# Kernel optimization log

Measured on AMD Instinct MI355X. Metric: run time of the kernel, lower is better.

## Reference

```python
import jax, jax.numpy as jnp
import numpy as np

N_GRAMS = 3
N_KERNELS = 11

def _kernel_mus(K):
    l = [1.0]
    if K == 1:
        return l
    bs = 2.0 / (K - 1)
    l.append(1.0 - bs / 2.0)
    for i in range(1, K - 1):
        l.append(l[i] - bs)
    return l

def _kernel_sigmas(K):
    if K == 1:
        return [0.001]
    bs = 2.0 / (K - 1)
    return [0.001] + [0.5 * bs] * (K - 1)

MU = jnp.asarray(_kernel_mus(N_KERNELS), jnp.float32)       # (K,)
SIGMA = jnp.asarray(_kernel_sigmas(N_KERNELS), jnp.float32)  # (K,)

def _conv_relu(x, w, b):
    # x: (B,E,L), w: (O,E,h); right-pad h-1 so output length == L (as ConstantPad1d((0,h-1)))
    h = w.shape[-1]
    y = jax.lax.conv_general_dilated(x, w, (1,), [(0, h - 1)], dimension_numbers=('NCH', 'OIH', 'NCH'))
    return jax.nn.relu(y + b[None, :, None]).transpose(0, 2, 1)  # (B,L,O)

def _cosine(a, b):
    # CosineMatrixAttention: normalize rows then matmul
    an = a / (jnp.linalg.norm(a, axis=-1, keepdims=True) + 1e-13)
    bn = b / (jnp.linalg.norm(b, axis=-1, keepdims=True) + 1e-13)
    return jnp.einsum('bqe,bde->bqd', an, bn)

def setup_inputs() -> dict:
    key = jax.random.key(0)
    ks = jax.random.split(key, 12)
    B, Lq, Ld, V, E, O = 128, 64, 512, 30000, 300, 128
    inp = {}
    inp['tokens_q'] = jax.random.randint(ks[0], (B, Lq), 0, V)
    inp['tokens_d'] = jax.random.randint(ks[1], (B, Ld), 0, V)
    inp['emb'] = jax.random.normal(ks[2], (V, E), jnp.float32) * 0.1
    for i, h in enumerate((1, 2, 3)):
        inp['conv_w%d' % h] = jax.random.normal(ks[3 + i], (O, E, h), jnp.float32) * (1.0 / np.sqrt(E * h))
        inp['conv_b%d' % h] = jnp.zeros((O,), jnp.float32)
    inp['fc_w'] = jax.random.normal(ks[9], (1, N_KERNELS * N_GRAMS * N_GRAMS), jnp.float32) * 0.1
    inp['fc_b'] = jnp.zeros((1,), jnp.float32)
    return inp

def reference(tokens_q, tokens_d, emb, conv_w1, conv_b1, conv_w2, conv_b2, conv_w3, conv_b3, fc_w, fc_b):
    qmask = (tokens_q > 0).astype(jnp.float32)  # (B,Lq)
    dmask = (tokens_d > 0).astype(jnp.float32)  # (B,Ld)
    qe = emb[tokens_q].transpose(0, 2, 1)  # (B,E,Lq)
    de = emb[tokens_d].transpose(0, 2, 1)  # (B,E,Ld)
    cws = [(conv_w1, conv_b1), (conv_w2, conv_b2), (conv_w3, conv_b3)]
    hq = [_conv_relu(qe, w, b) for w, b in cws]  # each (B,Lq,O)
    hd = [_conv_relu(de, w, b) for w, b in cws]  # each (B,Ld,O)
    pair_mask = qmask[:, :, None] * dmask[:, None, :]  # (B,Lq,Ld)
    mu = MU[None, None, None, :]
    sig = SIGMA[None, None, None, :]
    feats = []
    for q in range(N_GRAMS):
        for d in range(N_GRAMS):
            m = _cosine(hq[q], hd[d]) * pair_mask  # (B,Lq,Ld)
            rbf = jnp.exp(-jnp.square(m[..., None] - mu) / (2.0 * jnp.square(sig))) * pair_mask[..., None]
            qk = rbf.sum(axis=2)  # (B,Lq,K)
            logk = jnp.log(jnp.maximum(qk, 1e-10)) * 0.01
            # NOTE: original has a typo (loq_ vs log_) so the query mask is NOT applied before summing
            feats.append(logk.sum(axis=1))  # (B,K)
    cross = jnp.concatenate(feats, axis=-1)  # (B, K*G*G)
    return cross @ fc_w.T + fc_b  # (B,1)
```

## Files before the change

### kernel.cpp

```cpp
#include <hip/hip_runtime.h>
#include <hip/hip_bf16.h>

typedef __attribute__((ext_vector_type(8))) short short8;
typedef __attribute__((ext_vector_type(4))) float f32x4;

#define E_DIM 300
#define NCH   128
#define NOUT  384
#define NCHUNK 30

#define APITCH 656
#define OPITCH 792

__device__ __forceinline__ unsigned short f2bf(float f) {
    unsigned int u = __float_as_uint(f);
    u += 0x7FFFu + ((u >> 16) & 1u);
    return (unsigned short)(u >> 16);
}

__global__ void pack_wb(const float* __restrict__ w1, const float* __restrict__ w2,
                        const float* __restrict__ w3, unsigned short* __restrict__ Wp) {
    int idx = blockIdx.x * 256 + threadIdx.x;
    if (idx >= NCHUNK * NOUT * 32) return;
    int ke = idx & 31;
    int n  = (idx >> 5) % NOUT;
    int c  = idx / (32 * NOUT);
    int s  = c / 10;
    int e  = (c % 10) * 32 + ke;
    int g  = n >> 7, o = n & 127, h = g + 1;
    float v = 0.0f;
    if (e < E_DIM && s < h) {
        const float* w = (g == 0) ? w1 : ((g == 1) ? w2 : w3);
        v = w[(o * E_DIM + e) * h + s];
    }
    Wp[idx] = f2bf(v);
}

__launch_bounds__(512, 4)
__global__ void conv_mfma(const int* __restrict__ tokens_q, const int* __restrict__ tokens_d,
                          const float* __restrict__ emb, const unsigned short* __restrict__ Wp,
                          const float* __restrict__ b1, const float* __restrict__ b2,
                          const float* __restrict__ b3,
                          unsigned short* __restrict__ hq, unsigned short* __restrict__ hd) {
    __shared__ __align__(16) char lds[64 * OPITCH];
    __shared__ float nrm[64 * 3];

    int bx   = blockIdx.x;
    int b    = bx / 9;
    int tile = bx % 9;
    int isq  = (tile == 0);
    int L    = isq ? 64 : 512;
    int t0   = isq ? 0 : (tile - 1) * 64;
    const int* toks = isq ? (tokens_q + b * 64) : (tokens_d + b * 512);
    int tid  = threadIdx.x;
    int lane = tid & 63;
    int wn   = tid >> 6;
    int lr   = lane & 15;
    int lg   = lane >> 4;

    if (tid < 192) nrm[tid] = 0.0f;

    const unsigned short* __restrict__ wpB = Wp + (size_t)(wn * 16 + lr) * 32 + lg * 8;
    short8 bb[2][3];
    #pragma unroll
    for (int g = 0; g < 3; ++g) {
        bb[0][g] = *(const short8*)(wpB + (size_t)(0 * NOUT + g * 128) * 32);
        bb[1][g] = *(const short8*)(wpB + (size_t)(1 * NOUT + g * 128) * 32);
    }

    for (int i = tid; i < 66 * 80; i += 512) {
        int r   = i / 80;
        int f4  = i - r * 80;
        ushort4 u = {0, 0, 0, 0};
        int pos = t0 + r;
        if (f4 < 75 && pos < L) {
            int tk = toks[pos];
            float4 v = *(const float4*)(emb + (size_t)tk * E_DIM + f4 * 4);
            u.x = f2bf(v.x); u.y = f2bf(v.y); u.z = f2bf(v.z); u.w = f2bf(v.w);
        }
        *(ushort4*)(lds + r * APITCH + f4 * 8) = u;
    }
    __syncthreads();

    f32x4 acc[4][3];
    #pragma unroll
    for (int i = 0; i < 4; ++i)
        #pragma unroll
        for (int g = 0; g < 3; ++g) acc[i][g] = (f32x4){0.f, 0.f, 0.f, 0.f};

    const char* abase = lds + lr * APITCH + lg * 16;

    #pragma unroll
    for (int c = 0; c < NCHUNK; ++c) {
        const int S  = (c >= 20) ? 2 : ((c >= 10) ? 1 : 0);
        const int ec = c - S * 10;
        short8 a[4];
        #pragma unroll
        for (int i = 0; i < 4; ++i)
            a[i] = *(const short8*)(abase + (i * 16 + S) * APITCH + ec * 64);
        #pragma unroll
        for (int i = 0; i < 4; ++i)
            #pragma unroll
            for (int g = S; g < 3; ++g)
                acc[i][g] = __builtin_amdgcn_mfma_f32_16x16x32_bf16(a[i], bb[c & 1][g], acc[i][g], 0, 0, 0);
        if (c < NCHUNK - 2) {
            const int S2 = ((c + 2) >= 20) ? 2 : (((c + 2) >= 10) ? 1 : 0);
            #pragma unroll
            for (int g = S2; g < 3; ++g)
                bb[c & 1][g] = *(const short8*)(wpB + (size_t)((c + 2) * NOUT + g * 128) * 32);
        }
    }

    #pragma unroll
    for (int g = 0; g < 3; ++g) {
        float bv = (g == 0 ? b1 : (g == 1 ? b2 : b3))[wn * 16 + lr];
        #pragma unroll
        for (int i = 0; i < 4; ++i)
            #pragma unroll
            for (int r = 0; r < 4; ++r) {
                float v = acc[i][g][r] + bv;
                v = v > 0.0f ? v : 0.0f;
                acc[i][g][r] = v;
                float s = v * v;
                s += __shfl_xor(s, 1, 16);
                s += __shfl_xor(s, 2, 16);
                s += __shfl_xor(s, 4, 16);
                s += __shfl_xor(s, 8, 16);
                if (lr == 0) atomicAdd(&nrm[(i * 16 + lg * 4 + r) * 3 + g], s);
            }
    }
    __syncthreads();

    unsigned short* os = (unsigned short*)lds;
    #pragma unroll
    for (int i = 0; i < 4; ++i)
        #pragma unroll
        for (int r = 0; r < 4; ++r) {
            int row = i * 16 + lg * 4 + r;
            #pragma unroll
            for (int g = 0; g < 3; ++g) {
                float inv = 1.0f / (sqrtf(nrm[row * 3 + g]) + 1e-13f);
                os[row * (OPITCH / 2) + g * 128 + wn * 16 + lr] = f2bf(acc[i][g][r] * inv);
            }
        }
    __syncthreads();

    unsigned short* outp = isq ? hq : hd;
    #pragma unroll
    for (int it = 0; it < 12; ++it) {
        int idx = it * 512 + tid;
        int row = idx / 96;
        int c8  = idx - row * 96;
        int g   = c8 >> 5;
        int ch  = (c8 & 31) * 4;
        uint2 v = *(const uint2*)(lds + row * OPITCH + c8 * 8);
        *(uint2*)&outp[((size_t)(g * 128 + b) * L + t0 + row) * NCH + ch] = v;
    }
}

#define QPITCH 136
__launch_bounds__(256, 3)
__global__ void sim_rbf(const unsigned short* __restrict__ hq,
                        const unsigned short* __restrict__ hd,
                        const int* __restrict__ tokens_q, const int* __restrict__ tokens_d,
                        float* __restrict__ cross) {
    __shared__ __align__(16) short qs[64 * QPITCH];
    __shared__ __align__(16) short ds2[2][64 * QPITCH];
    __shared__ unsigned char dm_s[512];
    __shared__ float logk_s[11];

    int bx = blockIdx.x;
    int b  = bx / 9;
    int p  = bx % 9;
    int gq = p / 3;
    int gd = p % 3;
    int tid = threadIdx.x;
    int lane = tid & 63;
    int wn   = tid >> 6;
    int lr   = lane & 15;
    int lg   = lane >> 4;

    if (tid < 11) logk_s[tid] = 0.0f;
    for (int i = tid; i < 512; i += 256)
        dm_s[i] = (tokens_d[b * 512 + i] > 0) ? 1 : 0;

    const unsigned short* qsrc = hq + ((size_t)(gq * 128 + b) * 64) * NCH;
    const unsigned short* dsrc = hd + ((size_t)(gd * 128 + b) * 512) * NCH;

    #pragma unroll
    for (int it = 0; it < 4; ++it) {
        int row  = it * 16 + (tid >> 4);
        int col8 = (tid & 15) * 8;
        *(uint4*)&qs[row * QPITCH + col8] = *(const uint4*)&qsrc[row * NCH + col8];
    }
    #pragma unroll
    for (int it = 0; it < 4; ++it) {
        int row  = it * 16 + (tid >> 4);
        int col8 = (tid & 15) * 8;
        *(uint4*)&ds2[0][row * QPITCH + col8] = *(const uint4*)&dsrc[row * NCH + col8];
    }
    __syncthreads();

    int q  = wn * 16 + lr;
    float qm = (tokens_q[b * 64 + q] > 0) ? 1.0f : 0.0f;

    short8 qf[4];
    #pragma unroll
    for (int ks = 0; ks < 4; ++ks)
        qf[ks] = *(const short8*)&qs[(wn * 16 + lr) * QPITCH + ks * 32 + lg * 8];

    float qk[11];
    #pragma unroll
    for (int k = 0; k < 11; ++k) qk[k] = 0.0f;

    const float C4 = 0.0183156389f;

    for (int ch = 0; ch < 8; ++ch) {
        int buf = ch & 1;
        uint4 r4[4];
        if (ch < 7) {
            #pragma unroll
            for (int it = 0; it < 4; ++it) {
                int row  = it * 16 + (tid >> 4);
                int col8 = (tid & 15) * 8;
                r4[it] = *(const uint4*)&dsrc[((size_t)(ch + 1) * 64 + row) * NCH + col8];
            }
        }

        #pragma unroll
        for (int mt = 0; mt < 4; ++mt) {
            f32x4 acc = (f32x4){0.f, 0.f, 0.f, 0.f};
            #pragma unroll
            for (int ks = 0; ks < 4; ++ks) {
                short8 a = *(const short8*)&ds2[buf][(mt * 16 + lr) * QPITCH + ks * 32 + lg * 8];
                acc = __builtin_amdgcn_mfma_f32_16x16x32_bf16(a, qf[ks], acc, 0, 0, 0);
            }
            uchar4 du = *(const uchar4*)&dm_s[ch * 64 + mt * 16 + lg * 4];
            float cv[4], cm[4];
            cm[0] = qm * (float)du.x; cm[1] = qm * (float)du.y;
            cm[2] = qm * (float)du.z; cm[3] = qm * (float)du.w;
            #pragma unroll
            for (int r = 0; r < 4; ++r) cv[r] = acc[r] * cm[r];

            float cmx = fmaxf(fmaxf(cv[0], cv[1]), fmaxf(cv[2], cv[3]));
            if (__any(cmx > 0.98f)) {
                #pragma unroll
                for (int r = 0; r < 4; ++r) {
                    if (cv[r] > 0.98f) {
                        float t0 = cv[r] - 1.0f;
                        qk[0] += __expf(-500000.0f * t0 * t0);
                    }
                }
            }
            #pragma unroll
            for (int r = 0; r < 4; ++r) {
                float c  = cv[r];
                float tA = c - 0.1f;
                float TA = __expf(-50.0f * tA * tA) * cm[r];
                float UA = __expf(20.0f * c - 4.0f);
                float tB = c + 0.1f;
                float TB = __expf(-50.0f * tB * tB) * cm[r];
                float UB = __expf(-20.0f * c - 4.0f);
                qk[5] += TA;
                TA *= UA; qk[4] += TA; UA *= C4;
                TA *= UA; qk[3] += TA; UA *= C4;
                TA *= UA; qk[2] += TA; UA *= C4;
                TA *= UA; qk[1] += TA;
                qk[6] += TB;
                TB *= UB; qk[7] += TB; UB *= C4;
                TB *= UB; qk[8] += TB; UB *= C4;
                TB *= UB; qk[9] += TB; UB *= C4;
                TB *= UB; qk[10] += TB;
            }
        }

        if (ch < 7) {
            #pragma unroll
            for (int it = 0; it < 4; ++it) {
                int row  = it * 16 + (tid >> 4);
                int col8 = (tid & 15) * 8;
                *(uint4*)&ds2[buf ^ 1][row * QPITCH + col8] = r4[it];
            }
        }
        __syncthreads();
    }

    #pragma unroll
    for (int k = 0; k < 11; ++k) {
        float v = qk[k];
        v += __shfl_xor(v, 16);
        v += __shfl_xor(v, 32);
        qk[k] = v;
    }
    if (lg == 0) {
        #pragma unroll
        for (int k = 0; k < 11; ++k) {
            float lv = __logf(fmaxf(qk[k], 1e-10f)) * 0.01f;
            atomicAdd(&logk_s[k], lv);
        }
    }
    __syncthreads();
    if (tid < 11) cross[b * 99 + p * 11 + tid] = logk_s[tid];
}

__global__ void fc_kernel(const float* __restrict__ cross, const float* __restrict__ fc_w,
                          const float* __restrict__ fc_b, float* __restrict__ out) {
    int b = threadIdx.x;
    float acc = fc_b[0];
    #pragma unroll 11
    for (int j = 0; j < 99; ++j) acc += cross[b * 99 + j] * fc_w[j];
    out[b] = acc;
}

extern "C" void kernel_launch(void* const* d_in, const int* in_sizes, int n_in,
                              void* d_out, int out_size, void* d_ws, size_t ws_size,
                              hipStream_t stream) {
    const int*   tq  = (const int*)d_in[0];
    const int*   td  = (const int*)d_in[1];
    const float* emb = (const float*)d_in[2];
    const float* w1  = (const float*)d_in[3];
    const float* cb1 = (const float*)d_in[4];
    const float* w2  = (const float*)d_in[5];
    const float* cb2 = (const float*)d_in[6];
    const float* w3  = (const float*)d_in[7];
    const float* cb3 = (const float*)d_in[8];
    const float* fcw = (const float*)d_in[9];
    const float* fcb = (const float*)d_in[10];

    char* ws = (char*)d_ws;
    unsigned short* Wp    = (unsigned short*)ws;
    float*          cross = (float*)(ws + 921600);
    unsigned short* hq    = (unsigned short*)(ws + 1048576);
    unsigned short* hd    = (unsigned short*)(ws + 8388608);

    hipLaunchKernelGGL(pack_wb, dim3(1440), dim3(256), 0, stream, w1, w2, w3, Wp);
    hipLaunchKernelGGL(conv_mfma, dim3(128 * 9), dim3(512), 0, stream,
                       tq, td, emb, Wp, cb1, cb2, cb3, hq, hd);
    hipLaunchKernelGGL(sim_rbf, dim3(128 * 9), dim3(256), 0, stream, hq, hd, tq, td, cross);
    hipLaunchKernelGGL(fc_kernel, dim3(1), dim3(128), 0, stream, cross, fcw, fcb, (float*)d_out);
}
```

Baseline: 207.1 us.

## Swizzle embedding LDS tile and gather rows with 8 threads each

Reworks the embedding gather in the conv kernel so each token row is handled by 8 threads that issue 9-10 independent float4 loads. The rows are stored into LDS with a 640-byte pitch and an XOR swizzle on the 16-byte column, replacing the padded 656-byte pitch, and the MFMA A-operand reads apply the same swizzle. The aim is more memory-level parallelism in the gather and fewer LDS bank conflicts. It also precomputes the reciprocal norms once per row/group instead of recomputing sqrt and divide in every thread, at the cost of one extra barrier.

```diff
diff --git a/kernel.cpp b/kernel.cpp
--- a/kernel.cpp
+++ b/kernel.cpp
@@ -9,7 +9,6 @@
 #define NOUT  384
 #define NCHUNK 30
 
-#define APITCH 656
 #define OPITCH 792
 
 __device__ __forceinline__ unsigned short f2bf(float f) {
@@ -68,17 +67,40 @@
         bb[1][g] = *(const short8*)(wpB + (size_t)(1 * NOUT + g * 128) * 32);
     }
 
-    for (int i = tid; i < 66 * 80; i += 512) {
-        int r   = i / 80;
-        int f4  = i - r * 80;
-        ushort4 u = {0, 0, 0, 0};
-        int pos = t0 + r;
-        if (f4 < 75 && pos < L) {
-            int tk = toks[pos];
-            float4 v = *(const float4*)(emb + (size_t)tk * E_DIM + f4 * 4);
-            u.x = f2bf(v.x); u.y = f2bf(v.y); u.z = f2bf(v.z); u.w = f2bf(v.w);
-        }
-        *(ushort4*)(lds + r * APITCH + f4 * 8) = u;
+    {
+        auto gather_row = [&](int r, int sl) {
+            int pos = t0 + r;
+            int tk  = (pos < L) ? toks[pos] : -1;
+            char* wbase = lds + r * 640;
+            int xr = (r & 7) << 4;
+            if (tk >= 0) {
+                const float* src = emb + (size_t)tk * E_DIM + sl * 4;
+                float4 v[9];
+                #pragma unroll
+                for (int k = 0; k < 9; ++k) v[k] = *(const float4*)(src + k * 32);
+                #pragma unroll
+                for (int k = 0; k < 9; ++k) {
+                    ushort4 u;
+                    u.x = f2bf(v[k].x); u.y = f2bf(v[k].y);
+                    u.z = f2bf(v[k].z); u.w = f2bf(v[k].w);
+                    *(ushort4*)(wbase + ((((sl + 8 * k) * 8)) ^ xr)) = u;
+                }
+                ushort4 u9 = {0, 0, 0, 0};
+                if (sl < 3) {
+                    float4 v9 = *(const float4*)(src + 9 * 32);
+                    u9.x = f2bf(v9.x); u9.y = f2bf(v9.y);
+                    u9.z = f2bf(v9.z); u9.w = f2bf(v9.w);
+                }
+                *(ushort4*)(wbase + ((((sl + 72) * 8)) ^ xr)) = u9;
+            } else {
+                ushort4 z = {0, 0, 0, 0};
+                #pragma unroll
+                for (int k = 0; k < 10; ++k)
+                    *(ushort4*)(wbase + ((((sl + 8 * k) * 8)) ^ xr)) = z;
+            }
+        };
+        gather_row(tid >> 3, tid & 7);
+        if (tid < 16) gather_row(64 + (tid >> 3), tid & 7);
     }
     __syncthreads();
 
@@ -87,8 +109,6 @@
     for (int i = 0; i < 4; ++i)
         #pragma unroll
         for (int g = 0; g < 3; ++g) acc[i][g] = (f32x4){0.f, 0.f, 0.f, 0.f};
-
-    const char* abase = lds + lr * APITCH + lg * 16;
 
     #pragma unroll
     for (int c = 0; c < NCHUNK; ++c) {
@@ -96,8 +116,11 @@
         const int ec = c - S * 10;
         short8 a[4];
         #pragma unroll
-        for (int i = 0; i < 4; ++i)
-            a[i] = *(const short8*)(abase + (i * 16 + S) * APITCH + ec * 64);
+        for (int i = 0; i < 4; ++i) {
+            int row = i * 16 + lr + S;
+            int byt = (ec * 64 + lg * 16) ^ ((row & 7) << 4);
+            a[i] = *(const short8*)(lds + row * 640 + byt);
+        }
         #pragma unroll
         for (int i = 0; i < 4; ++i)
             #pragma unroll
@@ -131,6 +154,9 @@
     }
     __syncthreads();
 
+    if (tid < 192) nrm[tid] = 1.0f / (sqrtf(nrm[tid]) + 1e-13f);
+    __syncthreads();
+
     unsigned short* os = (unsigned short*)lds;
     #pragma unroll
     for (int i = 0; i < 4; ++i)
@@ -138,10 +164,8 @@
         for (int r = 0; r < 4; ++r) {
             int row = i * 16 + lg * 4 + r;
             #pragma unroll
-            for (int g = 0; g < 3; ++g) {
-                float inv = 1.0f / (sqrtf(nrm[row * 3 + g]) + 1e-13f);
-                os[row * (OPITCH / 2) + g * 128 + wn * 16 + lr] = f2bf(acc[i][g][r] * inv);
-            }
+            for (int g = 0; g < 3; ++g)
+                os[row * (OPITCH / 2) + g * 128 + wn * 16 + lr] = f2bf(acc[i][g][r] * nrm[row * 3 + g]);
         }
     __syncthreads();
 
```

After: 185.9 us. 10.2% less time.
